# Optimization experiments

Hardware: AMD Instinct MI355X
Metric: run time of the kernel (lower is better)

The kernel has to match this reference:

```python
import jax, jax.numpy as jnp
import numpy as np

B, D_MODEL, H = 2048, 1024, 16
D_K = D_MODEL // H


def setup_inputs() -> dict:
    root = jax.random.key(0)
    ks = jax.random.split(root, 11)
    w_scale = 1.0 / np.sqrt(D_MODEL).astype(np.float32)
    inp = {
        "query": jax.random.normal(ks[0], (B, D_MODEL), jnp.float32),
        "key": jax.random.normal(ks[1], (B, D_MODEL), jnp.float32),
        "value": jax.random.normal(ks[2], (B, D_MODEL), jnp.float32),
        # Linear weights (used as x @ W + b)
        "Wq": jax.random.normal(ks[3], (D_MODEL, D_MODEL), jnp.float32) * w_scale,
        "bq": jnp.zeros((D_MODEL,), jnp.float32),
        "Wk": jax.random.normal(ks[4], (D_MODEL, D_MODEL), jnp.float32) * w_scale,
        "bk": jnp.zeros((D_MODEL,), jnp.float32),
        "Wv": jax.random.normal(ks[5], (D_MODEL, D_MODEL), jnp.float32) * w_scale,
        "bv": jnp.zeros((D_MODEL,), jnp.float32),
        # Random U drawn fresh each forward in torch; materialized here for determinism.
        # torch shape: randn(d_model, nbatches*d_k).view(nbatches, h, d_k, d_k)
        "U": jax.random.normal(ks[6], (B, H, D_K, D_K), jnp.float32),
    }
    return inp


def reference(query, key, value, Wq, bq, Wk, bk, Wv, bv, U):
    b, dm = query.shape
    h = U.shape[1]
    dk = dm // h
    residual = key
    # QKV projections, then view(b, -1, h, dk).transpose(1, 2) -> [b, h, 1, dk]
    q = (query @ Wq + bq).reshape(b, 1, h, dk).transpose(0, 2, 1, 3)
    k = (key @ Wk + bk).reshape(b, 1, h, dk).transpose(0, 2, 1, 3)
    v = (value @ Wv + bv).reshape(b, 1, h, dk).transpose(0, 2, 1, 3)
    # attn_weight = (q @ U) @ k^T : [b,h,1,dk] @ [b,h,dk,dk] @ [b,h,dk,1] -> [b,h,1,1]
    aw = jnp.matmul(q, U)
    scores = jnp.matmul(aw, jnp.swapaxes(k, -1, -2))
    p = jax.nn.softmax(scores, axis=-1)  # dropout is identity at inference
    # context = p^T @ v : [b,h,1,1] @ [b,h,1,dk] -> [b,h,1,dk]
    ctx = jnp.matmul(jnp.swapaxes(p, -1, -2), v)
    ctx = jnp.swapaxes(ctx, 1, 2).reshape(b, dm)
    return ctx + residual
```

## Files before the change

kernel.cpp:

```cpp
#include <hip/hip_runtime.h>
#include <hip/hip_bf16.h>


#define M_DIM 2048
#define N_DIM 1024
#define K_DIM 1024

typedef __attribute__((ext_vector_type(8))) short short8;
typedef __attribute__((ext_vector_type(4))) float f32x4;

__device__ inline unsigned rne_bf16(float f) {
    unsigned u = __builtin_bit_cast(unsigned, f);
    return (u + 0x7FFFu + ((u >> 16) & 1u)) >> 16;
}
__device__ inline unsigned pack2(float lo, float hi) {
    return rne_bf16(lo) | (rne_bf16(hi) << 16);
}
__device__ inline void gl_lds16(const short* g, short* l) {
    __builtin_amdgcn_global_load_lds((const __attribute__((address_space(1))) void*)g,
                                     (__attribute__((address_space(3))) void*)l,
                                     16, 0, 0);
}

__global__ __launch_bounds__(256)
void convert_kernel(const float* __restrict__ value, const float* __restrict__ Wv,
                    short* __restrict__ Vb, short* __restrict__ WvTb) {
    __shared__ unsigned tr[64 * 36];
    const int b = blockIdx.x, tid = threadIdx.x;
    if (b < 1024) {
        int g = b * 256 + tid;
        int row = g >> 7, ch = g & 127;
        int kt = ch >> 3, c = ch & 7;
        int tm = row >> 6, r = row & 63;
        const float* p = value + (size_t)row * K_DIM + ch * 8;
        f32x4 a0 = *(const f32x4*)p;
        f32x4 a1 = *(const f32x4*)(p + 4);
        union { short8 s; unsigned u[4]; } o;
        o.u[0] = pack2(a0[0], a0[1]);
        o.u[1] = pack2(a0[2], a0[3]);
        o.u[2] = pack2(a1[0], a1[1]);
        o.u[3] = pack2(a1[2], a1[3]);
        *(short8*)&Vb[(size_t)(tm * 16 + kt) * 4096 + r * 64 + ((c ^ (r & 7)) << 3)] = o.s;
    } else {
        int b2 = b - 1024;
        int tn = b2 & 15, kt = b2 >> 4;
        #pragma unroll
        for (int s = 0; s < 2; ++s) {
            int kp = (tid >> 4) + s * 16;
            int n4 = (tid & 15) * 4;
            const float* bp = Wv + (size_t)(kt * 64 + 2 * kp) * N_DIM + tn * 64 + n4;
            f32x4 b0 = *(const f32x4*)bp;
            f32x4 b1 = *(const f32x4*)(bp + N_DIM);
            #pragma unroll
            for (int m = 0; m < 4; ++m)
                tr[(n4 + m) * 36 + kp] = pack2(b0[m], b1[m]);
        }
        __syncthreads();
        int n = tid >> 2;
        #pragma unroll
        for (int h = 0; h < 2; ++h) {
            int c = (tid & 3) + 4 * h;
            union { short8 s; unsigned u[4]; } o;
            #pragma unroll
            for (int p = 0; p < 4; ++p)
                o.u[p] = tr[n * 36 + c * 4 + p];
            *(short8*)&WvTb[(size_t)(tn * 16 + kt) * 4096 + n * 64 + ((c ^ (n & 7)) << 3)] = o.s;
        }
    }
}

__global__ __launch_bounds__(512)
void gemm_kernel(const short* __restrict__ Vb, const short* __restrict__ WvTb,
                 const float* __restrict__ key, const float* __restrict__ bv,
                 float* __restrict__ out) {
    __shared__ __align__(16) short As[4][8192];
    __shared__ __align__(16) short Bs[4][4096];

    const int tid = threadIdx.x;
    const int bid = blockIdx.x;
    const int xcd = bid & 7, idx = bid >> 3;
    const int bm2 = xcd * 2 + (idx >> 4);
    const int bn  = idx & 15;
    const int lane = tid & 63;
    const int wid = tid >> 6;
    const int wr = wid >> 1;
    const int wc = wid & 1;

    const short* Ab0 = Vb + (size_t)(bm2 * 2) * 16 * 4096;
    const short* Ab1 = Vb + (size_t)(bm2 * 2 + 1) * 16 * 4096;
    const short* Bb  = WvTb + (size_t)bn * 16 * 4096;
    const int row0 = bm2 * 128, col0 = bn * 64;

    f32x4 acc[2][2] = {};

    auto stage = [&](int buf, int kt) {
        gl_lds16(Ab0 + (size_t)kt * 4096 + tid * 8, &As[buf][tid * 8]);
        gl_lds16(Ab1 + (size_t)kt * 4096 + tid * 8, &As[buf][4096 + tid * 8]);
        gl_lds16(Bb  + (size_t)kt * 4096 + tid * 8, &Bs[buf][tid * 8]);
    };

    auto compute = [&](int buf) {
        #pragma unroll
        for (int ks = 0; ks < 2; ++ks) {
            short8 afr[2], bfr[2];
            const int g = ks * 4 + (lane >> 4);
            #pragma unroll
            for (int fm = 0; fm < 2; ++fm) {
                int r = wr * 32 + fm * 16 + (lane & 15);
                afr[fm] = *(const short8*)&As[buf][r * 64 + ((g ^ (r & 7)) << 3)];
            }
            #pragma unroll
            for (int fn = 0; fn < 2; ++fn) {
                int n = wc * 32 + fn * 16 + (lane & 15);
                bfr[fn] = *(const short8*)&Bs[buf][n * 64 + ((g ^ (n & 7)) << 3)];
            }
            #pragma unroll
            for (int fm = 0; fm < 2; ++fm)
                #pragma unroll
                for (int fn = 0; fn < 2; ++fn)
                    acc[fm][fn] = __builtin_amdgcn_mfma_f32_16x16x32_bf16(
                        afr[fm], bfr[fn], acc[fm][fn], 0, 0, 0);
        }
    };

    stage(0, 0);
    stage(1, 1);
    stage(2, 2);

    #pragma unroll
    for (int kt = 0; kt < 16; ++kt) {
        if (kt <= 13)      asm volatile("s_waitcnt vmcnt(6)" ::: "memory");
        else if (kt == 14) asm volatile("s_waitcnt vmcnt(3)" ::: "memory");
        else               asm volatile("s_waitcnt vmcnt(0)" ::: "memory");
        __builtin_amdgcn_s_barrier();
        if (kt + 3 < 16) stage((kt + 3) & 3, kt + 3);
        compute(kt & 3);
    }

    __syncthreads();
    float* T = (float*)&As[0][0];
    #pragma unroll
    for (int fm = 0; fm < 2; ++fm)
        #pragma unroll
        for (int fn = 0; fn < 2; ++fn) {
            int c = wc * 32 + fn * 16 + (lane & 15);
            #pragma unroll
            for (int i = 0; i < 4; ++i) {
                int r = wr * 32 + fm * 16 + (lane >> 4) * 4 + i;
                T[r * 68 + c] = acc[fm][fn][i];
            }
        }
    __syncthreads();
    #pragma unroll
    for (int it = 0; it < 4; ++it) {
        int r = it * 32 + (tid >> 4);
        int q = tid & 15;
        f32x4 vv = *(f32x4*)&T[r * 68 + q * 4];
        int grow = row0 + r, gcol = col0 + q * 4;
        f32x4 kv = *(const f32x4*)&key[(size_t)grow * N_DIM + gcol];
        f32x4 bb = *(const f32x4*)&bv[gcol];
        vv = vv + kv + bb;
        *(f32x4*)&out[(size_t)grow * N_DIM + gcol] = vv;
    }
}

extern "C" void kernel_launch(void* const* d_in, const int* in_sizes, int n_in,
                              void* d_out, int out_size, void* d_ws, size_t ws_size,
                              hipStream_t stream) {
    const float* key   = (const float*)d_in[1];
    const float* value = (const float*)d_in[2];
    const float* Wv    = (const float*)d_in[7];
    const float* bv    = (const float*)d_in[8];
    float* out = (float*)d_out;

    short* Vb   = (short*)d_ws;
    short* WvTb = (short*)d_ws + (size_t)M_DIM * K_DIM;

    convert_kernel<<<1024 + 256, 256, 0, stream>>>(value, Wv, Vb, WvTb);
    gemm_kernel<<<256, 512, 0, stream>>>(Vb, WvTb, key, bv, out);
}
```

Before: 22.33 us.

## Fuse fp32-to-bf16 conversion into GEMM with register-staged double-buffered loads

Removes the separate conversion kernel and its bf16 workspace round trip. The GEMM now loads fp32 value and Wv tiles straight into registers, converts and transposes them in registers, and writes swizzled bf16 tiles into double-buffered LDS. Register prefetching runs two tiles ahead, and the epilogue's key and bias loads are issued early. The cost is that each block re-converts shared operand data, pipeline depth drops from async 4-stage to register 2-stage, and the B-operand swizzle changes.

```diff
diff --git a/kernel.cpp b/kernel.cpp
--- a/kernel.cpp
+++ b/kernel.cpp
@@ -16,89 +16,68 @@
 __device__ inline unsigned pack2(float lo, float hi) {
     return rne_bf16(lo) | (rne_bf16(hi) << 16);
 }
-__device__ inline void gl_lds16(const short* g, short* l) {
-    __builtin_amdgcn_global_load_lds((const __attribute__((address_space(1))) void*)g,
-                                     (__attribute__((address_space(3))) void*)l,
-                                     16, 0, 0);
-}
-
-__global__ __launch_bounds__(256)
-void convert_kernel(const float* __restrict__ value, const float* __restrict__ Wv,
-                    short* __restrict__ Vb, short* __restrict__ WvTb) {
-    __shared__ unsigned tr[64 * 36];
-    const int b = blockIdx.x, tid = threadIdx.x;
-    if (b < 1024) {
-        int g = b * 256 + tid;
-        int row = g >> 7, ch = g & 127;
-        int kt = ch >> 3, c = ch & 7;
-        int tm = row >> 6, r = row & 63;
-        const float* p = value + (size_t)row * K_DIM + ch * 8;
-        f32x4 a0 = *(const f32x4*)p;
-        f32x4 a1 = *(const f32x4*)(p + 4);
-        union { short8 s; unsigned u[4]; } o;
-        o.u[0] = pack2(a0[0], a0[1]);
-        o.u[1] = pack2(a0[2], a0[3]);
-        o.u[2] = pack2(a1[0], a1[1]);
-        o.u[3] = pack2(a1[2], a1[3]);
-        *(short8*)&Vb[(size_t)(tm * 16 + kt) * 4096 + r * 64 + ((c ^ (r & 7)) << 3)] = o.s;
-    } else {
-        int b2 = b - 1024;
-        int tn = b2 & 15, kt = b2 >> 4;
-        #pragma unroll
-        for (int s = 0; s < 2; ++s) {
-            int kp = (tid >> 4) + s * 16;
-            int n4 = (tid & 15) * 4;
-            const float* bp = Wv + (size_t)(kt * 64 + 2 * kp) * N_DIM + tn * 64 + n4;
-            f32x4 b0 = *(const f32x4*)bp;
-            f32x4 b1 = *(const f32x4*)(bp + N_DIM);
-            #pragma unroll
-            for (int m = 0; m < 4; ++m)
-                tr[(n4 + m) * 36 + kp] = pack2(b0[m], b1[m]);
-        }
-        __syncthreads();
-        int n = tid >> 2;
-        #pragma unroll
-        for (int h = 0; h < 2; ++h) {
-            int c = (tid & 3) + 4 * h;
-            union { short8 s; unsigned u[4]; } o;
-            #pragma unroll
-            for (int p = 0; p < 4; ++p)
-                o.u[p] = tr[n * 36 + c * 4 + p];
-            *(short8*)&WvTb[(size_t)(tn * 16 + kt) * 4096 + n * 64 + ((c ^ (n & 7)) << 3)] = o.s;
-        }
-    }
-}
 
 __global__ __launch_bounds__(512)
-void gemm_kernel(const short* __restrict__ Vb, const short* __restrict__ WvTb,
-                 const float* __restrict__ key, const float* __restrict__ bv,
-                 float* __restrict__ out) {
-    __shared__ __align__(16) short As[4][8192];
-    __shared__ __align__(16) short Bs[4][4096];
+void fused_gemm(const float* __restrict__ value, const float* __restrict__ Wv,
+                const float* __restrict__ key, const float* __restrict__ bv,
+                float* __restrict__ out) {
+    __shared__ __align__(16) char smem[49152];
+    short (*As)[8192] = (short (*)[8192])smem;
+    short (*Bs)[4096] = (short (*)[4096])(smem + 32768);
 
-    const int tid = threadIdx.x;
-    const int bid = blockIdx.x;
+    const int tid = threadIdx.x, bid = blockIdx.x;
     const int xcd = bid & 7, idx = bid >> 3;
     const int bm2 = xcd * 2 + (idx >> 4);
     const int bn  = idx & 15;
-    const int lane = tid & 63;
-    const int wid = tid >> 6;
-    const int wr = wid >> 1;
-    const int wc = wid & 1;
+    const int row0 = bm2 * 128, col0 = bn * 64;
+    const int lane = tid & 63, wid = tid >> 6;
+    const int wr = wid >> 1, wc = wid & 1;
 
-    const short* Ab0 = Vb + (size_t)(bm2 * 2) * 16 * 4096;
-    const short* Ab1 = Vb + (size_t)(bm2 * 2 + 1) * 16 * 4096;
-    const short* Bb  = WvTb + (size_t)bn * 16 * 4096;
-    const int row0 = bm2 * 128, col0 = bn * 64;
+    const int rowA = tid >> 2;
+    const int kq   = tid & 3;
+    const float* aptr = value + (size_t)(row0 + rowA) * K_DIM + kq * 16;
+    const int kp = tid >> 4;
+    const int n4 = (tid & 15) * 4;
+    const float* bptr = Wv + (size_t)(2 * kp) * N_DIM + col0 + n4;
+
+    f32x4 sa[2][4];
+    f32x4 sb[2][2];
+
+    auto loadT = [&](int s, int kt) {
+        const float* ap = aptr + kt * 64;
+        sa[s][0] = *(const f32x4*)(ap + 0);
+        sa[s][1] = *(const f32x4*)(ap + 4);
+        sa[s][2] = *(const f32x4*)(ap + 8);
+        sa[s][3] = *(const f32x4*)(ap + 12);
+        const float* bp = bptr + (size_t)kt * 64 * N_DIM;
+        sb[s][0] = *(const f32x4*)bp;
+        sb[s][1] = *(const f32x4*)(bp + N_DIM);
+    };
+
+    auto cvtWrite = [&](int s, int buf) {
+        union { short8 v; unsigned u[4]; } c0, c1;
+        c0.u[0] = pack2(sa[s][0][0], sa[s][0][1]);
+        c0.u[1] = pack2(sa[s][0][2], sa[s][0][3]);
+        c0.u[2] = pack2(sa[s][1][0], sa[s][1][1]);
+        c0.u[3] = pack2(sa[s][1][2], sa[s][1][3]);
+        c1.u[0] = pack2(sa[s][2][0], sa[s][2][1]);
+        c1.u[1] = pack2(sa[s][2][2], sa[s][2][3]);
+        c1.u[2] = pack2(sa[s][3][0], sa[s][3][1]);
+        c1.u[3] = pack2(sa[s][3][2], sa[s][3][3]);
+        const int sw = rowA & 7;
+        *(short8*)&As[buf][rowA * 64 + (((kq * 2)     ^ sw) << 3)] = c0.v;
+        *(short8*)&As[buf][rowA * 64 + (((kq * 2 + 1) ^ sw) << 3)] = c1.v;
+        unsigned* bu = (unsigned*)&Bs[buf][0];
+        #pragma unroll
+        for (int m = 0; m < 4; ++m) {
+            unsigned u = pack2(sb[s][0][m], sb[s][1][m]);
+            int n = n4 + m;
+            int chB = (kp >> 2) ^ ((n >> 1) & 7);
+            bu[n * 32 + (chB << 2) + (kp & 3)] = u;
+        }
+    };
 
     f32x4 acc[2][2] = {};
-
-    auto stage = [&](int buf, int kt) {
-        gl_lds16(Ab0 + (size_t)kt * 4096 + tid * 8, &As[buf][tid * 8]);
-        gl_lds16(Ab1 + (size_t)kt * 4096 + tid * 8, &As[buf][4096 + tid * 8]);
-        gl_lds16(Bb  + (size_t)kt * 4096 + tid * 8, &Bs[buf][tid * 8]);
-    };
-
     auto compute = [&](int buf) {
         #pragma unroll
         for (int ks = 0; ks < 2; ++ks) {
@@ -112,7 +91,7 @@
             #pragma unroll
             for (int fn = 0; fn < 2; ++fn) {
                 int n = wc * 32 + fn * 16 + (lane & 15);
-                bfr[fn] = *(const short8*)&Bs[buf][n * 64 + ((g ^ (n & 7)) << 3)];
+                bfr[fn] = *(const short8*)&Bs[buf][n * 64 + ((g ^ ((n >> 1) & 7)) << 3)];
             }
             #pragma unroll
             for (int fm = 0; fm < 2; ++fm)
@@ -123,22 +102,36 @@
         }
     };
 
-    stage(0, 0);
-    stage(1, 1);
-    stage(2, 2);
+    f32x4 kr[4];
+    f32x4 br;
+    const int rE = tid >> 4;
+    const int cE = (tid & 15) * 4;
+
+    loadT(0, 0);
+    loadT(1, 1);
+    cvtWrite(0, 0);
+    asm volatile("s_waitcnt lgkmcnt(0)" ::: "memory");
+    __builtin_amdgcn_s_barrier();
+    __builtin_amdgcn_sched_barrier(0);
 
     #pragma unroll
     for (int kt = 0; kt < 16; ++kt) {
-        if (kt <= 13)      asm volatile("s_waitcnt vmcnt(6)" ::: "memory");
-        else if (kt == 14) asm volatile("s_waitcnt vmcnt(3)" ::: "memory");
-        else               asm volatile("s_waitcnt vmcnt(0)" ::: "memory");
+        const int buf = kt & 1;
+        if (kt + 2 < 16) loadT(buf, kt + 2);
+        compute(buf);
+        if (kt + 1 < 16) cvtWrite((kt + 1) & 1, buf ^ 1);
+        if (kt == 13) {
+            #pragma unroll
+            for (int it = 0; it < 4; ++it)
+                kr[it] = *(const f32x4*)&key[(size_t)(row0 + it * 32 + rE) * N_DIM + col0 + cE];
+            br = *(const f32x4*)&bv[col0 + cE];
+        }
+        asm volatile("s_waitcnt lgkmcnt(0)" ::: "memory");
         __builtin_amdgcn_s_barrier();
-        if (kt + 3 < 16) stage((kt + 3) & 3, kt + 3);
-        compute(kt & 3);
+        __builtin_amdgcn_sched_barrier(0);
     }
 
-    __syncthreads();
-    float* T = (float*)&As[0][0];
+    float* T = (float*)smem;
     #pragma unroll
     for (int fm = 0; fm < 2; ++fm)
         #pragma unroll
@@ -150,17 +143,14 @@
                 T[r * 68 + c] = acc[fm][fn][i];
             }
         }
-    __syncthreads();
+    asm volatile("s_waitcnt lgkmcnt(0)" ::: "memory");
+    __builtin_amdgcn_s_barrier();
     #pragma unroll
     for (int it = 0; it < 4; ++it) {
-        int r = it * 32 + (tid >> 4);
-        int q = tid & 15;
-        f32x4 vv = *(f32x4*)&T[r * 68 + q * 4];
-        int grow = row0 + r, gcol = col0 + q * 4;
-        f32x4 kv = *(const f32x4*)&key[(size_t)grow * N_DIM + gcol];
-        f32x4 bb = *(const f32x4*)&bv[gcol];
-        vv = vv + kv + bb;
-        *(f32x4*)&out[(size_t)grow * N_DIM + gcol] = vv;
+        int r = it * 32 + rE;
+        f32x4 vv = *(f32x4*)&T[r * 68 + cE];
+        vv = vv + kr[it] + br;
+        *(f32x4*)&out[(size_t)(row0 + r) * N_DIM + col0 + cE] = vv;
     }
 }
 
@@ -173,9 +163,5 @@
     const float* bv    = (const float*)d_in[8];
     float* out = (float*)d_out;
 
-    short* Vb   = (short*)d_ws;
-    short* WvTb = (short*)d_ws + (size_t)M_DIM * K_DIM;
-
-    convert_kernel<<<1024 + 256, 256, 0, stream>>>(value, Wv, Vb, WvTb);
-    gemm_kernel<<<256, 512, 0, stream>>>(Vb, WvTb, key, bv, out);
+    fused_gemm<<<256, 512, 0, stream>>>(value, Wv, key, bv, out);
 }
```

Result: faster. 21.43 us (-4.0%).
